# Optimization experiments

Hardware: AMD Instinct MI355X
Metric: run time of the kernel (lower is better)

Reference implementation:

```python
import jax, jax.numpy as jnp
import numpy as np

K = 2048      # codebook_size
D = 64        # codebook_dim
B = 32
T = 4096
W = 0.99      # codebook_loss_weight (EMA decay)
THRESH = 1.0  # discard_vec_threshold


def setup_inputs() -> dict:
    key = jax.random.key(0)
    k1, k2 = jax.random.split(key, 2)
    x = jax.random.normal(k1, (B, D, T), jnp.float32)
    codebook = jax.random.normal(k2, (K, D), jnp.float32)
    codebook_avg = codebook.copy()
    vector_usage = jnp.ones((K,), jnp.float32)
    perm = jnp.arange(B * T, dtype=jnp.int32)  # deterministic stand-in for randperm
    return dict(x=x, codebook=codebook, codebook_avg=codebook_avg,
                vector_usage=vector_usage, perm=perm)


def reference(x, codebook, codebook_avg, vector_usage, perm):
    Bv, E, Tv = x.shape
    sg = jax.lax.stop_gradient
    # preprocess: [B, E, T] -> [N, E]
    xf = jnp.transpose(x, (0, 2, 1)).reshape(-1, E)
    N = xf.shape[0]
    x_norm = jnp.linalg.norm(xf - jnp.mean(xf)) / np.sqrt(N * E)
    # squared euclidean distances [N, K]
    d = (jnp.sum(xf * xf, axis=-1, keepdims=True)
         - 2.0 * (xf @ codebook.T)
         + jnp.sum(codebook * codebook, axis=-1))
    idx = jnp.argmin(d, axis=-1)            # [N]
    fit = jnp.mean(jnp.min(d, axis=-1))
    q = codebook[idx]                       # [N, E] gather
    # --- update_codebook (torch.no_grad) ---
    cb_sum = jax.ops.segment_sum(sg(xf), idx, num_segments=K)          # onehot @ x
    counts = jax.ops.segment_sum(jnp.ones((N,), xf.dtype), idx, num_segments=K)
    new_avg = W * sg(codebook_avg) + (1.0 - W) * cb_sum
    new_usage = W * sg(vector_usage) + (1.0 - W) * counts
    keep = (new_usage >= THRESH).astype(xf.dtype)[:, None]
    random_shift = sg(xf)[perm][:K]
    new_codebook = keep * (new_avg / new_usage[:, None]) + (1.0 - keep) * random_shift
    vector_prob = counts / jnp.sum(counts)
    entropy = -jnp.sum(vector_prob * jnp.log(vector_prob + 1e-8))
    codebook_diff = jnp.linalg.norm(new_codebook - sg(codebook)) / np.sqrt(K * E)
    # --- commitment loss + straight-through ---
    commit_loss = jnp.sum((sg(q) - xf) ** 2) / (N * E)
    out = xf + sg(q - xf)
    out = jnp.transpose(out.reshape(Bv, Tv, E), (0, 2, 1))  # [B, E, T]
    return (out, commit_loss, fit, x_norm, new_codebook, new_avg, new_usage,
            entropy, codebook_diff)
```

## Files before the change

### kernel.cpp

```cpp
#include <hip/hip_runtime.h>
#include <math.h>

#define OUT_X      0
#define OUT_COMMIT 8388608
#define OUT_FIT    8388609
#define OUT_XNORM  8388610
#define OUT_NCB    8388611
#define OUT_NAVG   (8388611 + 131072)
#define OUT_NUSE   (8388611 + 262144)
#define OUT_ENT    (8388611 + 264192)
#define OUT_CBDIFF (8388611 + 264193)

#define WS_DACC    0
#define WS_COUNTS  64
#define WS_CBSUM   8256
#define WS_CURS    532544
#define WS_XN2     540736
#define WS_IDX     1065024
#define WS_CN2     1589312
#define WS_SORTED  1597504
#define WS_CHI     2121792
#define WS_CLO     2383936
#define WS_XT      2646080
#define WS_XT_END  (2646080 + 33554432)
#define WS_ZERO_BYTES 532544

#define LO_SCALE   2048.0f
#define LO_INV     4.8828125e-4f

typedef _Float16 f16x8_t __attribute__((ext_vector_type(8)));
typedef float f32x16_t __attribute__((ext_vector_type(16)));

__device__ __forceinline__ void gload_lds16(const _Float16* g, _Float16* l) {
    __builtin_amdgcn_global_load_lds(
        (const __attribute__((address_space(1))) unsigned int*)(g),
        (__attribute__((address_space(3))) unsigned int*)(l), 16, 0, 0);
}

__global__ __launch_bounds__(256) void kern_prep_x(
    const float* __restrict__ x, float* __restrict__ xt,
    float* __restrict__ xn2, double* __restrict__ dacc)
{
    __shared__ __align__(16) float Xs[64][128];
    __shared__ float tmpA[4], tmpB[4];
    const int tid = threadIdx.x;
    const int n0 = blockIdx.x * 128;
    const int b = n0 >> 12, t0 = n0 & 4095;
    const float* xb = x + ((size_t)b << 18) + t0;
#pragma unroll
    for (int i = 0; i < 8; ++i) {
        int c = i * 256 + tid;
        int e = c >> 5, v4 = c & 31;
        float4 f = *(const float4*)(xb + ((size_t)e << 12) + (v4 << 2));
        *(float4*)&Xs[e][v4 << 2] = f;
    }
    __syncthreads();
    const int q = tid & 3, r0 = tid >> 2;
    float s1t = 0.f, s2t = 0.f;
#pragma unroll
    for (int h = 0; h < 2; ++h) {
        int r = r0 + (h << 6);
        float s2 = 0.f;
#pragma unroll
        for (int j = 0; j < 4; ++j) {
            int e = q * 16 + j * 4;
            float4 f = make_float4(Xs[e][r], Xs[e + 1][r], Xs[e + 2][r], Xs[e + 3][r]);
            *(float4*)(xt + (((size_t)(n0 + r)) << 6) + e) = f;
            s1t += f.x + f.y + f.z + f.w;
            s2 += f.x * f.x + f.y * f.y + f.z * f.z + f.w * f.w;
        }
        s2t += s2;
        float s2q = s2 + __shfl_xor(s2, 1, 64);
        s2q += __shfl_xor(s2q, 2, 64);
        if (q == 0) xn2[n0 + r] = s2q;
    }
    float rs = s1t, r2 = s2t;
#pragma unroll
    for (int m = 32; m >= 1; m >>= 1) {
        rs += __shfl_xor(rs, m, 64);
        r2 += __shfl_xor(r2, m, 64);
    }
    if ((tid & 63) == 0) { tmpA[tid >> 6] = rs; tmpB[tid >> 6] = r2; }
    __syncthreads();
    if (tid == 0) {
        atomicAdd(&dacc[0], (double)(tmpA[0] + tmpA[1] + tmpA[2] + tmpA[3]));
        atomicAdd(&dacc[1], (double)(tmpB[0] + tmpB[1] + tmpB[2] + tmpB[3]));
    }
}

__global__ __launch_bounds__(256) void kern_prep_cb(
    const float* __restrict__ cb, _Float16* __restrict__ chi,
    _Float16* __restrict__ clo, float* __restrict__ cn2)
{
    __shared__ float Cs[128][68];
    const int tid = threadIdx.x;
    const int c0 = blockIdx.x * 128;
#pragma unroll
    for (int i = 0; i < 8; ++i) {
        int li = i * 256 + tid;
        int code = li >> 4, d4 = li & 15;
        float4 f = *(const float4*)(cb + (((size_t)(c0 + code)) << 6) + (d4 << 2));
        Cs[code][d4 * 4 + 0] = f.x; Cs[code][d4 * 4 + 1] = f.y;
        Cs[code][d4 * 4 + 2] = f.z; Cs[code][d4 * 4 + 3] = f.w;
    }
    __syncthreads();
    const int w = tid >> 6, lane = tid & 63;
    const int cl = (w << 5) + (lane & 31);
    const int g = lane >> 5;
    const int ktg = blockIdx.x * 4 + w;
#pragma unroll
    for (int s = 0; s < 4; ++s) {
        f16x8_t hh, ll;
#pragma unroll
        for (int i = 0; i < 8; ++i) {
            int k = 16 * s + 4 * g + (i & 3) + 8 * (i >> 2);
            float v = Cs[cl][k];
            _Float16 h = (_Float16)v;
            hh[i] = h;
            ll[i] = (_Float16)((v - (float)h) * LO_SCALE);
        }
        *(f16x8_t*)(chi + (((size_t)(ktg * 4 + s)) << 9) + lane * 8) = hh;
        *(f16x8_t*)(clo + (((size_t)(ktg * 4 + s)) << 9) + lane * 8) = ll;
    }
    if (tid < 128) {
        float s = 0.f;
#pragma unroll
        for (int k = 0; k < 64; ++k) { float v = Cs[tid][k]; s = fmaf(v, v, s); }
        cn2[c0 + tid] = s;
    }
}

__global__ __launch_bounds__(256) void kern_argmin_mfma(
    const float* __restrict__ x, const float* __restrict__ cn2,
    const _Float16* __restrict__ chi, const _Float16* __restrict__ clo,
    const float* __restrict__ xn2, int* __restrict__ idxb,
    unsigned* __restrict__ counts, double* __restrict__ dacc)
{
    __shared__ __align__(16) _Float16 Bs[2][8][512];
    const int tid = threadIdx.x;
    const int w = tid >> 6, lane = tid & 63;
    const int n0 = blockIdx.x * 128 + w * 32;
    const int b = n0 >> 12, t0 = n0 & 4095;
    const int col = lane & 31, g = lane >> 5;

    f16x8_t ahi[4], alo[4];
    {
        const float* xb = x + ((size_t)b << 18) + t0 + col;
#pragma unroll
        for (int s = 0; s < 4; ++s) {
#pragma unroll
            for (int i = 0; i < 8; ++i) {
                int k = 16 * s + 4 * g + (i & 3) + 8 * (i >> 2);
                float v = xb[(size_t)k << 12];
                _Float16 h = (_Float16)v;
                ahi[s][i] = h;
                alo[s][i] = (_Float16)((v - (float)h) * LO_SCALE);
            }
        }
    }
    float minv[16]; int minkt[16];
#pragma unroll
    for (int r = 0; r < 16; ++r) { minv[r] = INFINITY; minkt[r] = 0; }

    {
        size_t off = ((size_t)w << 9) + lane * 8;
        gload_lds16(chi + off, &Bs[0][w * 2 + 0][0]);
        gload_lds16(clo + off, &Bs[0][w * 2 + 1][0]);
    }
    __syncthreads();
    int buf = 0;
    for (int kt = 0; kt < 64; ++kt) {
        if (kt + 1 < 64) {
            size_t off = (((size_t)(kt + 1) * 4 + w) << 9) + lane * 8;
            gload_lds16(chi + off, &Bs[buf ^ 1][w * 2 + 0][0]);
            gload_lds16(clo + off, &Bs[buf ^ 1][w * 2 + 1][0]);
        }
        float cv = cn2[(kt << 5) + col];
        f32x16_t am, ac;
#pragma unroll
        for (int r = 0; r < 16; ++r) { am[r] = 0.f; ac[r] = 0.f; }
#pragma unroll
        for (int s = 0; s < 4; ++s) {
            f16x8_t bh = *(const f16x8_t*)&Bs[buf][s * 2 + 0][lane * 8];
            f16x8_t bl = *(const f16x8_t*)&Bs[buf][s * 2 + 1][lane * 8];
            ac = __builtin_amdgcn_mfma_f32_32x32x16_f16(alo[s], bh, ac, 0, 0, 0);
            ac = __builtin_amdgcn_mfma_f32_32x32x16_f16(ahi[s], bl, ac, 0, 0, 0);
            am = __builtin_amdgcn_mfma_f32_32x32x16_f16(ahi[s], bh, am, 0, 0, 0);
        }
#pragma unroll
        for (int r = 0; r < 16; ++r) {
            float dot = fmaf(LO_INV, ac[r], am[r]);
            float d = fmaf(-2.f, dot, cv);
            if (d < minv[r]) { minv[r] = d; minkt[r] = kt; }
        }
        __syncthreads();
        buf ^= 1;
    }
    float fs = 0.f;
#pragma unroll
    for (int r = 0; r < 16; ++r) {
        float mv = minv[r]; int mi = (minkt[r] << 5) + col;
#pragma unroll
        for (int m = 1; m < 32; m <<= 1) {
            float ov = __shfl_xor(mv, m, 64);
            int oi = __shfl_xor(mi, m, 64);
            if (ov < mv || (ov == mv && oi < mi)) { mv = ov; mi = oi; }
        }
        if (col == 0) {
            int row = (r & 3) + 8 * (r >> 2) + 4 * g;
            int n = n0 + row;
            idxb[n] = mi;
            atomicAdd(&counts[mi], 1u);
            fs += xn2[n] + mv;
        }
    }
    if (col == 0) atomicAdd(&dacc[2], (double)fs);
}

__global__ void kern_scan(const unsigned* __restrict__ counts, unsigned* __restrict__ curs) {
    __shared__ unsigned wtot[4];
    const int tid = threadIdx.x;
    const int base = tid * 8;
    unsigned s[8]; unsigned tot = 0;
#pragma unroll
    for (int j = 0; j < 8; ++j) { s[j] = counts[base + j]; tot += s[j]; }
    unsigned v = tot;
    const int lane = tid & 63;
#pragma unroll
    for (int d = 1; d < 64; d <<= 1) {
        unsigned o = (unsigned)__shfl_up((int)v, d, 64);
        if (lane >= d) v += o;
    }
    if (lane == 63) wtot[tid >> 6] = v;
    __syncthreads();
    unsigned wbase = 0;
    for (int w = 0; w < (tid >> 6); ++w) wbase += wtot[w];
    unsigned run = wbase + v - tot;
#pragma unroll
    for (int j = 0; j < 8; ++j) { curs[base + j] = run; run += s[j]; }
}

__global__ void kern_scatter(const int* __restrict__ idxb, unsigned* __restrict__ curs,
                             unsigned* __restrict__ sorted) {
    const int n = blockIdx.x * 256 + threadIdx.x;
    int k = idxb[n];
    unsigned pos = atomicAdd(&curs[k], 1u);
    sorted[pos] = ((unsigned)k << 17) | (unsigned)n;
}

__global__ __launch_bounds__(256) void kern_chunk_reduce(
    const float* __restrict__ xt, const unsigned* __restrict__ sorted,
    float* __restrict__ cb_sum)
{
    const int tid = threadIdx.x;
    const int w = tid >> 6, lane = tid & 63;
    const int base = blockIdx.x * 256 + w * 64;
    int kcur = (int)(sorted[base] >> 17);
    float acc = 0.f;
#pragma unroll 4
    for (int it = 0; it < 16; ++it) {
        uint4 p = *(const uint4*)&sorted[base + it * 4];
        float v0 = xt[((size_t)(p.x & 0x1FFFFu) << 6) + lane];
        float v1 = xt[((size_t)(p.y & 0x1FFFFu) << 6) + lane];
        float v2 = xt[((size_t)(p.z & 0x1FFFFu) << 6) + lane];
        float v3 = xt[((size_t)(p.w & 0x1FFFFu) << 6) + lane];
        int k0 = (int)(p.x >> 17), k1 = (int)(p.y >> 17);
        int k2 = (int)(p.z >> 17), k3 = (int)(p.w >> 17);
        if (k0 != kcur) { atomicAdd(&cb_sum[(kcur << 6) + lane], acc); kcur = k0; acc = 0.f; }
        acc += v0;
        if (k1 != kcur) { atomicAdd(&cb_sum[(kcur << 6) + lane], acc); kcur = k1; acc = 0.f; }
        acc += v1;
        if (k2 != kcur) { atomicAdd(&cb_sum[(kcur << 6) + lane], acc); kcur = k2; acc = 0.f; }
        acc += v2;
        if (k3 != kcur) { atomicAdd(&cb_sum[(kcur << 6) + lane], acc); kcur = k3; acc = 0.f; }
        acc += v3;
    }
    atomicAdd(&cb_sum[(kcur << 6) + lane], acc);
}

__global__ __launch_bounds__(256) void kern_update(
    const float* __restrict__ cb_sum, const unsigned* __restrict__ counts,
    const float* __restrict__ cb, const float* __restrict__ cba,
    const float* __restrict__ usage, const int* __restrict__ perm,
    const float* __restrict__ xt, float* __restrict__ out,
    double* __restrict__ dacc)
{
    const int tid = threadIdx.x;
    const int i = blockIdx.x * 256 + tid;
    const int k = i >> 6, e = i & 63;
    float na = 0.99f * cba[i] + 0.01f * cb_sum[i];
    float nu = 0.99f * usage[k] + 0.01f * (float)counts[k];
    float ncb = (nu >= 1.0f) ? (na / nu)
                             : xt[((size_t)perm[k] << 6) + e];
    out[OUT_NAVG + i] = na;
    out[OUT_NCB + i] = ncb;
    if (e == 0) out[OUT_NUSE + k] = nu;
    float d = ncb - cb[i];
    float dd = d * d;
#pragma unroll
    for (int m = 32; m >= 1; m >>= 1) dd += __shfl_xor(dd, m, 64);
    if (e == 0) atomicAdd(&dacc[4], (double)dd);
}

__global__ __launch_bounds__(256) void kern_out(
    const float* __restrict__ x, const float* __restrict__ cb,
    const int* __restrict__ idxb, float* __restrict__ out,
    double* __restrict__ dacc) {
    __shared__ float tmp[4];
    const int tid = threadIdx.x;
    const int n0 = blockIdx.x * 256 + (tid & 63) * 4;
    const int ec = tid >> 6;
    const int b = n0 >> 12, t = n0 & 4095;
    int4 k4 = *(const int4*)(idxb + n0);
    const float* xb = x + ((size_t)b << 18) + t;
    float* ob = out + OUT_X + ((size_t)b << 18) + t;
    float cl = 0.f;
#pragma unroll
    for (int j = 0; j < 16; ++j) {
        int e = ec * 16 + j;
        float4 xv = *(const float4*)(xb + ((size_t)e << 12));
        float q0 = cb[((size_t)k4.x << 6) + e], q1 = cb[((size_t)k4.y << 6) + e];
        float q2 = cb[((size_t)k4.z << 6) + e], q3 = cb[((size_t)k4.w << 6) + e];
        float r0 = q0 - xv.x, r1 = q1 - xv.y, r2 = q2 - xv.z, r3 = q3 - xv.w;
        cl += r0 * r0 + r1 * r1 + r2 * r2 + r3 * r3;
        *(float4*)(ob + ((size_t)e << 12)) = make_float4(q0, q1, q2, q3);
    }
#pragma unroll
    for (int m = 32; m >= 1; m >>= 1) cl += __shfl_xor(cl, m, 64);
    if ((tid & 63) == 0) tmp[tid >> 6] = cl;
    __syncthreads();
    if (tid == 0) atomicAdd(&dacc[3], (double)(tmp[0] + tmp[1] + tmp[2] + tmp[3]));
}

__global__ void kern_scalars(const unsigned* __restrict__ counts,
                             const double* __restrict__ dacc, float* __restrict__ out) {
    __shared__ float tmp[4];
    __shared__ float totalSh;
    const int tid = threadIdx.x;
    float c = 0.f;
    for (int k = tid; k < 2048; k += 256) c += (float)counts[k];
#pragma unroll
    for (int m = 32; m >= 1; m >>= 1) c += __shfl_xor(c, m, 64);
    if ((tid & 63) == 0) tmp[tid >> 6] = c;
    __syncthreads();
    if (tid == 0) totalSh = tmp[0] + tmp[1] + tmp[2] + tmp[3];
    __syncthreads();
    const float total = totalSh;
    float ent = 0.f;
    for (int k = tid; k < 2048; k += 256) {
        float p = (float)counts[k] / total;
        ent -= p * logf(p + 1e-8f);
    }
#pragma unroll
    for (int m = 32; m >= 1; m >>= 1) ent += __shfl_xor(ent, m, 64);
    __syncthreads();
    if ((tid & 63) == 0) tmp[tid >> 6] = ent;
    __syncthreads();
    if (tid == 0) {
        float entropy = tmp[0] + tmp[1] + tmp[2] + tmp[3];
        out[OUT_COMMIT] = (float)(dacc[3] / 8388608.0);
        out[OUT_FIT]    = (float)(dacc[2] / 131072.0);
        double nd = 8388608.0;
        double var = dacc[1] - dacc[0] * dacc[0] / nd;
        if (var < 0.0) var = 0.0;
        out[OUT_XNORM] = (float)(sqrt(var) / sqrt(nd));
        out[OUT_ENT] = entropy;
        out[OUT_CBDIFF] = (float)(sqrt(dacc[4]) / sqrt(131072.0));
    }
}

extern "C" void kernel_launch(void* const* d_in, const int* in_sizes, int n_in,
                              void* d_out, int out_size, void* d_ws, size_t ws_size,
                              hipStream_t stream) {
    const float* x     = (const float*)d_in[0];
    const float* cb    = (const float*)d_in[1];
    const float* cba   = (const float*)d_in[2];
    const float* usage = (const float*)d_in[3];
    const int*   perm  = (const int*)d_in[4];
    float* out = (float*)d_out;
    char* ws = (char*)d_ws;
    double*    dacc   = (double*)(ws + WS_DACC);
    unsigned*  counts = (unsigned*)(ws + WS_COUNTS);
    float*     cbsum  = (float*)(ws + WS_CBSUM);
    unsigned*  curs   = (unsigned*)(ws + WS_CURS);
    float*     xn2    = (float*)(ws + WS_XN2);
    int*       idxb   = (int*)(ws + WS_IDX);
    float*     cn2    = (float*)(ws + WS_CN2);
    unsigned*  sorted = (unsigned*)(ws + WS_SORTED);
    _Float16*  chi    = (_Float16*)(ws + WS_CHI);
    _Float16*  clo    = (_Float16*)(ws + WS_CLO);
    float* xt = (ws_size >= (size_t)WS_XT_END) ? (float*)(ws + WS_XT) : (out + OUT_X);

    hipMemsetAsync(ws, 0, WS_ZERO_BYTES, stream);
    kern_prep_x<<<1024, 256, 0, stream>>>(x, xt, xn2, dacc);
    kern_prep_cb<<<16, 256, 0, stream>>>(cb, chi, clo, cn2);
    kern_argmin_mfma<<<1024, 256, 0, stream>>>(x, cn2, chi, clo, xn2, idxb, counts, dacc);
    kern_scan<<<1, 256, 0, stream>>>(counts, curs);
    kern_scatter<<<512, 256, 0, stream>>>(idxb, curs, sorted);
    kern_chunk_reduce<<<512, 256, 0, stream>>>(xt, sorted, cbsum);
    kern_update<<<512, 256, 0, stream>>>(cbsum, counts, cb, cba, usage, perm, xt, out, dacc);
    kern_out<<<512, 256, 0, stream>>>(x, cb, idxb, out, dacc);
    kern_scalars<<<1, 256, 0, stream>>>(counts, dacc, out);
}
```

Measured before the change: 296.7 us.

## Fold codebook norm into MFMA accumulator and double code tiles per barrier

The argmin kernel now preloads -0.5*||c||^2 into the main accumulator and tracks a running max of the dot product, which drops the per-element -2x FMA. It processes two 32-code tiles per sync, with a larger LDS double buffer and launch bounds requesting 4 blocks per CU. The x fragments are read as float4 from the transposed copy instead of strided scalar loads. That transposed copy now always lives in the output buffer rather than the optional workspace region, and the larger LDS footprint may reduce occupancy.

```diff
diff --git a/kernel.cpp b/kernel.cpp
--- a/kernel.cpp
+++ b/kernel.cpp
@@ -17,12 +17,10 @@
 #define WS_CURS    532544
 #define WS_XN2     540736
 #define WS_IDX     1065024
-#define WS_CN2     1589312
+#define WS_CN2H    1589312
 #define WS_SORTED  1597504
 #define WS_CHI     2121792
 #define WS_CLO     2383936
-#define WS_XT      2646080
-#define WS_XT_END  (2646080 + 33554432)
 #define WS_ZERO_BYTES 532544
 
 #define LO_SCALE   2048.0f
@@ -90,7 +88,7 @@
 
 __global__ __launch_bounds__(256) void kern_prep_cb(
     const float* __restrict__ cb, _Float16* __restrict__ chi,
-    _Float16* __restrict__ clo, float* __restrict__ cn2)
+    _Float16* __restrict__ clo, float* __restrict__ cn2h)
 {
     __shared__ float Cs[128][68];
     const int tid = threadIdx.x;
@@ -126,72 +124,81 @@
         float s = 0.f;
 #pragma unroll
         for (int k = 0; k < 64; ++k) { float v = Cs[tid][k]; s = fmaf(v, v, s); }
-        cn2[c0 + tid] = s;
-    }
-}
-
-__global__ __launch_bounds__(256) void kern_argmin_mfma(
-    const float* __restrict__ x, const float* __restrict__ cn2,
+        cn2h[c0 + tid] = -0.5f * s;
+    }
+}
+
+__global__ __launch_bounds__(256, 4) void kern_argmin_mfma(
+    const float* __restrict__ xt, const float* __restrict__ cn2h,
     const _Float16* __restrict__ chi, const _Float16* __restrict__ clo,
     const float* __restrict__ xn2, int* __restrict__ idxb,
     unsigned* __restrict__ counts, double* __restrict__ dacc)
 {
-    __shared__ __align__(16) _Float16 Bs[2][8][512];
+    __shared__ __align__(16) _Float16 Bs[2][2][8][512];
     const int tid = threadIdx.x;
     const int w = tid >> 6, lane = tid & 63;
     const int n0 = blockIdx.x * 128 + w * 32;
-    const int b = n0 >> 12, t0 = n0 & 4095;
-    const int col = lane & 31, g = lane >> 5;
+    const int l31 = lane & 31, g = lane >> 5;
 
     f16x8_t ahi[4], alo[4];
     {
-        const float* xb = x + ((size_t)b << 18) + t0 + col;
+        const float* xr = xt + ((size_t)(n0 + l31) << 6) + 4 * g;
 #pragma unroll
         for (int s = 0; s < 4; ++s) {
+            float4 p = *(const float4*)(xr + 16 * s);
+            float4 q = *(const float4*)(xr + 16 * s + 8);
+            float vals[8] = {p.x, p.y, p.z, p.w, q.x, q.y, q.z, q.w};
 #pragma unroll
             for (int i = 0; i < 8; ++i) {
-                int k = 16 * s + 4 * g + (i & 3) + 8 * (i >> 2);
-                float v = xb[(size_t)k << 12];
-                _Float16 h = (_Float16)v;
+                _Float16 h = (_Float16)vals[i];
                 ahi[s][i] = h;
-                alo[s][i] = (_Float16)((v - (float)h) * LO_SCALE);
+                alo[s][i] = (_Float16)((vals[i] - (float)h) * LO_SCALE);
             }
         }
     }
-    float minv[16]; int minkt[16];
-#pragma unroll
-    for (int r = 0; r < 16; ++r) { minv[r] = INFINITY; minkt[r] = 0; }
-
-    {
-        size_t off = ((size_t)w << 9) + lane * 8;
-        gload_lds16(chi + off, &Bs[0][w * 2 + 0][0]);
-        gload_lds16(clo + off, &Bs[0][w * 2 + 1][0]);
+    float bestm[16]; int besti[16];
+#pragma unroll
+    for (int r = 0; r < 16; ++r) { bestm[r] = -INFINITY; besti[r] = 0; }
+
+#pragma unroll
+    for (int j = 0; j < 4; ++j) {
+        int seg = (j << 2) | w;
+        int tt = seg >> 3, sh = seg & 7;
+        size_t off = (((size_t)(0 * 2 + tt) * 4 + (sh >> 1)) << 9) + lane * 8;
+        gload_lds16(((sh & 1) ? clo : chi) + off, &Bs[0][tt][sh][0]);
     }
     __syncthreads();
     int buf = 0;
-    for (int kt = 0; kt < 64; ++kt) {
-        if (kt + 1 < 64) {
-            size_t off = (((size_t)(kt + 1) * 4 + w) << 9) + lane * 8;
-            gload_lds16(chi + off, &Bs[buf ^ 1][w * 2 + 0][0]);
-            gload_lds16(clo + off, &Bs[buf ^ 1][w * 2 + 1][0]);
-        }
-        float cv = cn2[(kt << 5) + col];
-        f32x16_t am, ac;
-#pragma unroll
-        for (int r = 0; r < 16; ++r) { am[r] = 0.f; ac[r] = 0.f; }
-#pragma unroll
-        for (int s = 0; s < 4; ++s) {
-            f16x8_t bh = *(const f16x8_t*)&Bs[buf][s * 2 + 0][lane * 8];
-            f16x8_t bl = *(const f16x8_t*)&Bs[buf][s * 2 + 1][lane * 8];
-            ac = __builtin_amdgcn_mfma_f32_32x32x16_f16(alo[s], bh, ac, 0, 0, 0);
-            ac = __builtin_amdgcn_mfma_f32_32x32x16_f16(ahi[s], bl, ac, 0, 0, 0);
-            am = __builtin_amdgcn_mfma_f32_32x32x16_f16(ahi[s], bh, am, 0, 0, 0);
-        }
-#pragma unroll
-        for (int r = 0; r < 16; ++r) {
-            float dot = fmaf(LO_INV, ac[r], am[r]);
-            float d = fmaf(-2.f, dot, cv);
-            if (d < minv[r]) { minv[r] = d; minkt[r] = kt; }
+    for (int kt2 = 0; kt2 < 32; ++kt2) {
+        if (kt2 + 1 < 32) {
+#pragma unroll
+            for (int j = 0; j < 4; ++j) {
+                int seg = (j << 2) | w;
+                int tt = seg >> 3, sh = seg & 7;
+                size_t off = (((size_t)(kt2 + 1) * 2 + tt) * 4 + (sh >> 1) << 9) + lane * 8;
+                gload_lds16(((sh & 1) ? clo : chi) + off, &Bs[buf ^ 1][tt][sh][0]);
+            }
+        }
+#pragma unroll
+        for (int tt = 0; tt < 2; ++tt) {
+            const int tg = kt2 * 2 + tt;
+            float cv = cn2h[(tg << 5) + l31];
+            f32x16_t am, ac;
+#pragma unroll
+            for (int r = 0; r < 16; ++r) { am[r] = cv; ac[r] = 0.f; }
+#pragma unroll
+            for (int s = 0; s < 4; ++s) {
+                f16x8_t bh = *(const f16x8_t*)&Bs[buf][tt][s * 2 + 0][lane * 8];
+                f16x8_t bl = *(const f16x8_t*)&Bs[buf][tt][s * 2 + 1][lane * 8];
+                ac = __builtin_amdgcn_mfma_f32_32x32x16_f16(alo[s], bh, ac, 0, 0, 0);
+                ac = __builtin_amdgcn_mfma_f32_32x32x16_f16(ahi[s], bl, ac, 0, 0, 0);
+                am = __builtin_amdgcn_mfma_f32_32x32x16_f16(ahi[s], bh, am, 0, 0, 0);
+            }
+#pragma unroll
+            for (int r = 0; r < 16; ++r) {
+                float m = fmaf(LO_INV, ac[r], am[r]);
+                if (m > bestm[r]) { bestm[r] = m; besti[r] = tg; }
+            }
         }
         __syncthreads();
         buf ^= 1;
@@ -199,22 +206,22 @@
     float fs = 0.f;
 #pragma unroll
     for (int r = 0; r < 16; ++r) {
-        float mv = minv[r]; int mi = (minkt[r] << 5) + col;
+        float mv = bestm[r]; int mi = (besti[r] << 5) + l31;
 #pragma unroll
         for (int m = 1; m < 32; m <<= 1) {
             float ov = __shfl_xor(mv, m, 64);
             int oi = __shfl_xor(mi, m, 64);
-            if (ov < mv || (ov == mv && oi < mi)) { mv = ov; mi = oi; }
-        }
-        if (col == 0) {
+            if (ov > mv || (ov == mv && oi < mi)) { mv = ov; mi = oi; }
+        }
+        if (l31 == 0) {
             int row = (r & 3) + 8 * (r >> 2) + 4 * g;
             int n = n0 + row;
             idxb[n] = mi;
             atomicAdd(&counts[mi], 1u);
-            fs += xn2[n] + mv;
-        }
-    }
-    if (col == 0) atomicAdd(&dacc[2], (double)fs);
+            fs += xn2[n] - 2.f * mv;
+        }
+    }
+    if (l31 == 0) atomicAdd(&dacc[2], (double)fs);
 }
 
 __global__ void kern_scan(const unsigned* __restrict__ counts, unsigned* __restrict__ curs) {
@@ -385,16 +392,16 @@
     unsigned*  curs   = (unsigned*)(ws + WS_CURS);
     float*     xn2    = (float*)(ws + WS_XN2);
     int*       idxb   = (int*)(ws + WS_IDX);
-    float*     cn2    = (float*)(ws + WS_CN2);
+    float*     cn2h   = (float*)(ws + WS_CN2H);
     unsigned*  sorted = (unsigned*)(ws + WS_SORTED);
     _Float16*  chi    = (_Float16*)(ws + WS_CHI);
     _Float16*  clo    = (_Float16*)(ws + WS_CLO);
-    float* xt = (ws_size >= (size_t)WS_XT_END) ? (float*)(ws + WS_XT) : (out + OUT_X);
+    float*     xt     = out + OUT_X;
 
     hipMemsetAsync(ws, 0, WS_ZERO_BYTES, stream);
     kern_prep_x<<<1024, 256, 0, stream>>>(x, xt, xn2, dacc);
-    kern_prep_cb<<<16, 256, 0, stream>>>(cb, chi, clo, cn2);
-    kern_argmin_mfma<<<1024, 256, 0, stream>>>(x, cn2, chi, clo, xn2, idxb, counts, dacc);
+    kern_prep_cb<<<16, 256, 0, stream>>>(cb, chi, clo, cn2h);
+    kern_argmin_mfma<<<1024, 256, 0, stream>>>(xt, cn2h, chi, clo, xn2, idxb, counts, dacc);
     kern_scan<<<1, 256, 0, stream>>>(counts, curs);
     kern_scatter<<<512, 256, 0, stream>>>(idxb, curs, sorted);
     kern_chunk_reduce<<<512, 256, 0, stream>>>(xt, sorted, cbsum);
```

New measurement: 292.9 us. Within noise of the previous version (-1.3%).
